# Optimization experiments

Hardware: AMD Instinct MI355X
Metric: run time of the kernel (lower is better)

Reference implementation:

```python
import jax, jax.numpy as jnp
import numpy as np

N, E, D_IN, D, HEADS = 8192, 2048, 256, 256, 4
EPS = 1e-5
NEG = -1e9  # large negative instead of -inf (rows guaranteed non-empty anyway)


def _layernorm(x, g, b):
    mu = jnp.mean(x, axis=-1, keepdims=True)
    var = jnp.mean(jnp.square(x - mu), axis=-1, keepdims=True)
    return (x - mu) * jax.lax.rsqrt(var + EPS) * g + b


def _mha(q_x, kv_x, in_w, in_b, out_w, out_b, mask):
    """torch nn.MultiheadAttention (batch=1, eval) with boolean attn_mask.
    q_x: [Lq, D], kv_x: [Lk, D], mask: [Lq, Lk] True = blocked."""
    hd = D // HEADS
    wq, wk, wv = jnp.split(in_w, 3, axis=0)   # each [D, D]
    bq, bk, bv = jnp.split(in_b, 3, axis=0)
    q = (q_x @ wq.T + bq).reshape(-1, HEADS, hd).transpose(1, 0, 2)  # [h, Lq, hd]
    k = (kv_x @ wk.T + bk).reshape(-1, HEADS, hd).transpose(1, 0, 2)
    v = (kv_x @ wv.T + bv).reshape(-1, HEADS, hd).transpose(1, 0, 2)
    scores = jnp.einsum('hqd,hkd->hqk', q, k) / jnp.sqrt(jnp.asarray(hd, q.dtype))
    scores = jnp.where(mask[None, :, :], NEG, scores)
    attn = jax.nn.softmax(scores, axis=-1)
    out = jnp.einsum('hqk,hkd->hqd', attn, v)           # [h, Lq, hd]
    out = out.transpose(1, 0, 2).reshape(-1, D)          # [Lq, D]
    return out @ out_w.T + out_b


def setup_inputs() -> dict:
    key = jax.random.key(0)
    ks = jax.random.split(key, 12)
    s = 0.02
    x_0 = jax.random.normal(ks[0], (N, D_IN), jnp.float32)
    x_1 = jax.random.normal(ks[1], (E, D_IN), jnp.float32)
    H = (jax.random.uniform(ks[2], (N, E)) < 0.01).astype(jnp.float32)
    H = H.at[jnp.arange(N), jnp.arange(N) % E].set(1.0)
    return {
        'x_0': x_0, 'x_1': x_1, 'incidence_1': H,
        'node_w': jax.random.normal(ks[3], (D, D_IN), jnp.float32) * s,
        'node_b': jnp.zeros((D,), jnp.float32),
        'edge_w': jax.random.normal(ks[4], (D, D_IN), jnp.float32) * s,
        'edge_b': jnp.zeros((D,), jnp.float32),
        'n2e_in_w': jax.random.normal(ks[5], (3 * D, D), jnp.float32) * s,
        'n2e_in_b': jnp.zeros((3 * D,), jnp.float32),
        'n2e_out_w': jax.random.normal(ks[6], (D, D), jnp.float32) * s,
        'n2e_out_b': jnp.zeros((D,), jnp.float32),
        'e2n_in_w': jax.random.normal(ks[7], (3 * D, D), jnp.float32) * s,
        'e2n_in_b': jnp.zeros((3 * D,), jnp.float32),
        'e2n_out_w': jax.random.normal(ks[8], (D, D), jnp.float32) * s,
        'e2n_out_b': jnp.zeros((D,), jnp.float32),
        'norm1_g': jnp.ones((D,), jnp.float32),
        'norm1_b': jnp.zeros((D,), jnp.float32),
        'norm2_g': jnp.ones((D,), jnp.float32),
        'norm2_b': jnp.zeros((D,), jnp.float32),
    }


def reference(x_0, x_1, incidence_1, node_w, node_b, edge_w, edge_b,
              n2e_in_w, n2e_in_b, n2e_out_w, n2e_out_b,
              e2n_in_w, e2n_in_b, e2n_out_w, e2n_out_b,
              norm1_g, norm1_b, norm2_g, norm2_b):
    H = incidence_1                      # [N, E]
    x_0_p = x_0 @ node_w.T + node_b      # [N, D]
    x_1_p = x_1 @ edge_w.T + edge_b      # [E, D]
    # node -> edge: edges query nodes, mask where H.T == 0
    x_1_u = _mha(x_1_p, x_0_p, n2e_in_w, n2e_in_b, n2e_out_w, n2e_out_b,
                 H.T == 0)
    x_1_u = _layernorm(x_1_p + x_1_u, norm1_g, norm1_b)
    # edge -> node: nodes query updated edges, mask where H == 0
    x_0_u = _mha(x_0_p, x_1_u, e2n_in_w, e2n_in_b, e2n_out_w, e2n_out_b,
                 H == 0)
    x_0_u = _layernorm(x_0_p + x_0_u, norm2_g, norm2_b)
    return (x_0_u, x_1_u)
```

## Files before the change

### kernel.cpp

```cpp
#include <hip/hip_runtime.h>
#include <hip/hip_bf16.h>

using bf16 = __hip_bfloat16;
typedef __attribute__((ext_vector_type(4))) float  f32x4;
typedef __attribute__((ext_vector_type(8))) short  s16x8;

#define QSTRIDE 1040
#define ASTRIDE 520
#define BSTRIDE 2064
#define CMAX 256
#define RMAX 128
#define CSTRIDE 16

struct ConvDesc { const float* src[14]; int dstoff[14]; int cnt[14]; };

__global__ __launch_bounds__(256)
void conv_weights(ConvDesc d, bf16* __restrict__ dst, int* __restrict__ cz, int czn)
{
    const int seg = blockIdx.x >> 6;
    const int blk = blockIdx.x & 63;
    if (seg == 14) {
        for (int i = blk * 256 + threadIdx.x; i < czn; i += 64 * 256)
            cz[i] = 0;
        return;
    }
    const float* __restrict__ s = d.src[seg];
    bf16* __restrict__ o = dst + d.dstoff[seg];
    const int n = d.cnt[seg];
    for (int i = blk * 256 + threadIdx.x; i < n; i += 64 * 256)
        o[i] = __float2bfloat16(s[i]);
}

__global__ __launch_bounds__(256)
void build_rows(const float* __restrict__ H, int* __restrict__ row_cnt,
                unsigned short* __restrict__ row_idx)
{
    const int lane = threadIdx.x & 63;
    const int n    = blockIdx.x * 4 + (threadIdx.x >> 6);

    const unsigned long long ltm = (1ull << lane) - 1ull;
    int base = 0;

#pragma unroll
    for (int seg = 0; seg < 8; seg++) {
        f32x4 v = *(const f32x4*)(H + (size_t)n * 2048 + seg * 256 + lane * 4);
        unsigned long long b[4];
#pragma unroll
        for (int j = 0; j < 4; j++) b[j] = __ballot(v[j] != 0.f);

        int pre = 0;
#pragma unroll
        for (int j = 0; j < 4; j++) {
            if (v[j] != 0.f) {
                const int slot = base + pre + (int)__popcll(b[j] & ltm);
                if (slot < RMAX)
                    row_idx[(size_t)n * RMAX + slot] =
                        (unsigned short)(seg * 256 + lane * 4 + j);
            }
            pre += (int)__popcll(b[j]);
        }
        base += pre;
    }
    if (lane == 0) row_cnt[n] = (base < RMAX) ? base : RMAX;
}

__global__ __launch_bounds__(256)
void build_cols(const int* __restrict__ row_cnt,
                const unsigned short* __restrict__ row_idx,
                int* __restrict__ col_cnt, unsigned short* __restrict__ col_idx)
{
    const int g = blockIdx.x * 256 + threadIdx.x;
    const int n = g >> 3;
    const int t = g & 7;
    const int cnt = row_cnt[n];
    for (int i = t; i < cnt; i += 8) {
        const int e = row_idx[(size_t)n * RMAX + i];
        const int s = atomicAdd(&col_cnt[e * CSTRIDE], 1);
        if (s < CMAX) col_idx[(size_t)e * CMAX + s] = (unsigned short)n;
    }
}

__global__ __launch_bounds__(256, 2)
void gemm_proj(const float* __restrict__ X0, const float* __restrict__ X1,
               const bf16* __restrict__ Wc, const bf16* __restrict__ biasc,
               bf16* __restrict__ outB)
{
    __shared__ __align__(16) bf16 As[4 * QSTRIDE];
    __shared__ __align__(16) bf16 Bs[4 * QSTRIDE];

    const int t    = threadIdx.x;
    const int lane = t & 63;
    const int w    = t >> 6;
    const int wm   = (w >> 1) * 64;
    const int wn   = (w & 1) * 64;
    const int bt   = blockIdx.x >> 1;
    const int tn   = (blockIdx.x & 1) * 128;
    if (bt >= 80) return;

    const float* __restrict__ A = (bt < 64) ? X0 : X1;
    const int arow = (bt < 64) ? bt * 128 : (bt - 64) * 128;
    const bf16* __restrict__ W    = Wc    + ((bt < 64) ? 0 : 65536);
    const bf16* __restrict__ bias = biasc + ((bt < 64) ? 0 : 256);
    const int tm = bt * 128;

    f32x4 acc[4][4];
#pragma unroll
    for (int i = 0; i < 4; i++)
#pragma unroll
        for (int j = 0; j < 4; j++)
#pragma unroll
            for (int r = 0; r < 4; r++) acc[i][j][r] = 0.f;

    const int m0 = t >> 2,         q0 = t & 3;
    const int m1 = (t + 256) >> 2, q1 = (t + 256) & 3;
    const int fq = lane >> 4, fr = lane & 15;

    for (int k0 = 0; k0 < 256; k0 += 32) {
        f32x4 a0l = *(const f32x4*)(A + (size_t)(arow + m0) * 256 + k0 + q0 * 8);
        f32x4 a0h = *(const f32x4*)(A + (size_t)(arow + m0) * 256 + k0 + q0 * 8 + 4);
        f32x4 a1l = *(const f32x4*)(A + (size_t)(arow + m1) * 256 + k0 + q1 * 8);
        f32x4 a1h = *(const f32x4*)(A + (size_t)(arow + m1) * 256 + k0 + q1 * 8 + 4);
        union { s16x8 v; bf16 e[8]; } u0, u1;
#pragma unroll
        for (int j = 0; j < 4; j++) {
            u0.e[j] = __float2bfloat16(a0l[j]); u0.e[4 + j] = __float2bfloat16(a0h[j]);
            u1.e[j] = __float2bfloat16(a1l[j]); u1.e[4 + j] = __float2bfloat16(a1h[j]);
        }
        s16x8 sb0 = *(const s16x8*)(W + (size_t)(tn + m0) * 256 + k0 + q0 * 8);
        s16x8 sb1 = *(const s16x8*)(W + (size_t)(tn + m1) * 256 + k0 + q1 * 8);

        __syncthreads();
        *(s16x8*)&As[q0 * QSTRIDE + m0 * 8] = u0.v;
        *(s16x8*)&As[q1 * QSTRIDE + m1 * 8] = u1.v;
        *(s16x8*)&Bs[q0 * QSTRIDE + m0 * 8] = sb0;
        *(s16x8*)&Bs[q1 * QSTRIDE + m1 * 8] = sb1;
        __syncthreads();

        s16x8 af[4], bfv[4];
#pragma unroll
        for (int i = 0; i < 4; i++) {
            af[i]  = *(const s16x8*)&As[fq * QSTRIDE + (wm + i * 16 + fr) * 8];
            bfv[i] = *(const s16x8*)&Bs[fq * QSTRIDE + (wn + i * 16 + fr) * 8];
        }
#pragma unroll
        for (int i = 0; i < 4; i++)
#pragma unroll
            for (int j = 0; j < 4; j++)
                acc[i][j] = __builtin_amdgcn_mfma_f32_16x16x32_bf16(
                    af[i], bfv[j], acc[i][j], 0, 0, 0);
    }

#pragma unroll
    for (int j = 0; j < 4; j++) {
        const int ncol = tn + wn + j * 16 + fr;
        const float bj = __bfloat162float(bias[ncol]);
#pragma unroll
        for (int i = 0; i < 4; i++)
#pragma unroll
            for (int r = 0; r < 4; r++) {
                const int mrow = tm + wm + i * 16 + fq * 4 + r;
                outB[(size_t)mrow * 256 + ncol] = __float2bfloat16(acc[i][j][r] + bj);
            }
    }
}

__global__ __launch_bounds__(256, 2)
void gemm_dual(const bf16* __restrict__ A0, const bf16* __restrict__ W0,
               const bf16* __restrict__ bias0, bf16* __restrict__ out0,
               int N0, int tiles0, int nblk0,
               const bf16* __restrict__ A1, const bf16* __restrict__ W1,
               const bf16* __restrict__ bias1, bf16* __restrict__ out1,
               int N1, int tiles1)
{
    __shared__ __align__(16) bf16 As[4 * QSTRIDE];
    __shared__ __align__(16) bf16 Bs[4 * QSTRIDE];

    const int t    = threadIdx.x;
    const int lane = t & 63;
    const int w    = t >> 6;
    const int wm   = (w >> 1) * 64;
    const int wn   = (w & 1) * 64;

    const bool second = (blockIdx.x >= (unsigned)nblk0);
    const int  bi     = second ? (blockIdx.x - nblk0) : blockIdx.x;
    const bf16* __restrict__ A    = second ? A1 : A0;
    const bf16* __restrict__ W    = second ? W1 : W0;
    const bf16* __restrict__ bias = second ? bias1 : bias0;
    bf16* __restrict__ outB       = second ? out1 : out0;
    const int N      = second ? N1 : N0;
    const int tilesN = second ? tiles1 : tiles0;
    const int tm = (bi / tilesN) * 128;
    const int tn = (bi % tilesN) * 128;

    f32x4 acc[4][4];
#pragma unroll
    for (int i = 0; i < 4; i++)
#pragma unroll
        for (int j = 0; j < 4; j++)
#pragma unroll
            for (int r = 0; r < 4; r++) acc[i][j][r] = 0.f;

    const int m0 = t >> 2,         q0 = t & 3;
    const int m1 = (t + 256) >> 2, q1 = (t + 256) & 3;
    const int fq = lane >> 4, fr = lane & 15;

    for (int k0 = 0; k0 < 256; k0 += 32) {
        s16x8 sa0 = *(const s16x8*)(A + (size_t)(tm + m0) * 256 + k0 + q0 * 8);
        s16x8 sa1 = *(const s16x8*)(A + (size_t)(tm + m1) * 256 + k0 + q1 * 8);
        s16x8 sb0 = *(const s16x8*)(W + (size_t)(tn + m0) * 256 + k0 + q0 * 8);
        s16x8 sb1 = *(const s16x8*)(W + (size_t)(tn + m1) * 256 + k0 + q1 * 8);

        __syncthreads();
        *(s16x8*)&As[q0 * QSTRIDE + m0 * 8] = sa0;
        *(s16x8*)&As[q1 * QSTRIDE + m1 * 8] = sa1;
        *(s16x8*)&Bs[q0 * QSTRIDE + m0 * 8] = sb0;
        *(s16x8*)&Bs[q1 * QSTRIDE + m1 * 8] = sb1;
        __syncthreads();

        s16x8 af[4], bfv[4];
#pragma unroll
        for (int i = 0; i < 4; i++) {
            af[i]  = *(const s16x8*)&As[fq * QSTRIDE + (wm + i * 16 + fr) * 8];
            bfv[i] = *(const s16x8*)&Bs[fq * QSTRIDE + (wn + i * 16 + fr) * 8];
        }
#pragma unroll
        for (int i = 0; i < 4; i++)
#pragma unroll
            for (int j = 0; j < 4; j++)
                acc[i][j] = __builtin_amdgcn_mfma_f32_16x16x32_bf16(
                    af[i], bfv[j], acc[i][j], 0, 0, 0);
    }

#pragma unroll
    for (int j = 0; j < 4; j++) {
        const int ncol = tn + wn + j * 16 + fr;
        const float bj = __bfloat162float(bias[ncol]);
#pragma unroll
        for (int i = 0; i < 4; i++)
#pragma unroll
            for (int r = 0; r < 4; r++) {
                const int mrow = tm + wm + i * 16 + fq * 4 + r;
                outB[(size_t)mrow * N + ncol] = __float2bfloat16(acc[i][j][r] + bj);
            }
    }
}

__global__ __launch_bounds__(256, 2)
void gemm_ln(const bf16* __restrict__ A, const bf16* __restrict__ W,
             const float* __restrict__ biasF, const bf16* __restrict__ xp,
             const float* __restrict__ g, const float* __restrict__ b,
             float* __restrict__ outF, bf16* __restrict__ outB)
{
    __shared__ __align__(16) bf16 As[4 * ASTRIDE];
    __shared__ __align__(16) bf16 Bs[4 * BSTRIDE];
    __shared__ float rs1[64], rs2[64];

    const int t    = threadIdx.x;
    const int lane = t & 63;
    const int w    = t >> 6;
    const int fq   = lane >> 4;
    const int fr   = lane & 15;
    const int tm   = blockIdx.x * 64;

    if (t < 64) { rs1[t] = 0.f; rs2[t] = 0.f; }

    f32x4 acc[4][4];
#pragma unroll
    for (int i = 0; i < 4; i++)
#pragma unroll
        for (int j = 0; j < 4; j++)
#pragma unroll
            for (int r = 0; r < 4; r++) acc[i][j][r] = 0.f;

    const int mA = t >> 2, qA = t & 3;

    for (int k0 = 0; k0 < 256; k0 += 32) {
        s16x8 sa = *(const s16x8*)(A + (size_t)(tm + mA) * 256 + k0 + qA * 8);
        s16x8 sb[4];
#pragma unroll
        for (int s = 0; s < 4; s++)
            sb[s] = *(const s16x8*)(W + (size_t)(mA + 64 * s) * 256 + k0 + qA * 8);

        __syncthreads();
        *(s16x8*)&As[qA * ASTRIDE + mA * 8] = sa;
#pragma unroll
        for (int s = 0; s < 4; s++)
            *(s16x8*)&Bs[qA * BSTRIDE + (mA + 64 * s) * 8] = sb[s];
        __syncthreads();

        s16x8 af[4], bfv[4];
#pragma unroll
        for (int i = 0; i < 4; i++) {
            af[i]  = *(const s16x8*)&As[fq * ASTRIDE + (i * 16 + fr) * 8];
            bfv[i] = *(const s16x8*)&Bs[fq * BSTRIDE + (w * 64 + i * 16 + fr) * 8];
        }
#pragma unroll
        for (int i = 0; i < 4; i++)
#pragma unroll
            for (int j = 0; j < 4; j++)
                acc[i][j] = __builtin_amdgcn_mfma_f32_16x16x32_bf16(
                    af[i], bfv[j], acc[i][j], 0, 0, 0);
    }

    float bj[4], gj[4], bbj[4];
    int colv[4];
#pragma unroll
    for (int j = 0; j < 4; j++) {
        colv[j] = w * 64 + j * 16 + fr;
        bj[j]  = biasF[colv[j]];
        gj[j]  = g[colv[j]];
        bbj[j] = b[colv[j]];
    }

#pragma unroll
    for (int i = 0; i < 4; i++) {
#pragma unroll
        for (int r = 0; r < 4; r++) {
            const int row = i * 16 + fq * 4 + r;
            float t1 = 0.f, t2 = 0.f;
#pragma unroll
            for (int j = 0; j < 4; j++) {
                float v = acc[i][j][r] + bj[j]
                        + __bfloat162float(xp[(size_t)(tm + row) * 256 + colv[j]]);
                acc[i][j][r] = v;
                t1 += v;
                t2 += v * v;
            }
#pragma unroll
            for (int o = 1; o < 16; o <<= 1) {
                t1 += __shfl_xor(t1, o);
                t2 += __shfl_xor(t2, o);
            }
            if (fr == 0) {
                atomicAdd(&rs1[row], t1);
                atomicAdd(&rs2[row], t2);
            }
        }
    }
    __syncthreads();

#pragma unroll
    for (int i = 0; i < 4; i++) {
#pragma unroll
        for (int r = 0; r < 4; r++) {
            const int row = i * 16 + fq * 4 + r;
            const float mu  = rs1[row] * (1.f / 256.f);
            const float var = rs2[row] * (1.f / 256.f) - mu * mu;
            const float rstd = rsqrtf(var + 1e-5f);
#pragma unroll
            for (int j = 0; j < 4; j++) {
                const float y = (acc[i][j][r] - mu) * rstd * gj[j] + bbj[j];
                outF[(size_t)(tm + row) * 256 + colv[j]] = y;
                if (outB) outB[(size_t)(tm + row) * 256 + colv[j]] = __float2bfloat16(y);
            }
        }
    }
}

__global__ __launch_bounds__(256)
void sparse_attn(const bf16* __restrict__ Q, int qs,
                 const bf16* __restrict__ Kb, const bf16* __restrict__ Vb, int kvs,
                 const int* __restrict__ cnts, int cstride,
                 const unsigned short* __restrict__ idx,
                 int lmax, int idxmask, bf16* __restrict__ out)
{
    __shared__ float sc[4][CMAX];
    __shared__ unsigned short nls[CMAX];
    const int qi   = blockIdx.x;
    const int h    = threadIdx.x >> 6;
    const int lane = threadIdx.x & 63;
    const int grp  = lane >> 3;
    const int sub  = lane & 7;

    int n = cnts[(size_t)qi * cstride];
    if (n > lmax) n = lmax;

    if (h == 0)
        for (int i = lane; i < n; i += 64)
            nls[i] = (unsigned short)(((int)idx[(size_t)qi * lmax + i]) & idxmask);
    __syncthreads();

    if (n <= 0) {
        out[(size_t)qi * 256 + h * 64 + lane] = __float2bfloat16(0.f);
        return;
    }

    float qv[8];
    {
        union { f32x4 v; unsigned short u[8]; } qu;
        qu.v = *(const f32x4*)(Q + (size_t)qi * qs + h * 64 + sub * 8);
#pragma unroll
        for (int j = 0; j < 8; j++)
            qv[j] = __uint_as_float(((unsigned)qu.u[j]) << 16) * 0.125f;
    }

    float mx = -1e30f;
#pragma unroll 2
    for (int base = 0; base < n; base += 8) {
        const int i = base + grp;
        float s = -1e30f;
        if (i < n) {
            const int nb = nls[i];
            union { f32x4 v; unsigned short u[8]; } ku;
            ku.v = *(const f32x4*)(Kb + (size_t)nb * kvs + h * 64 + sub * 8);
            float a = 0.f;
#pragma unroll
            for (int j = 0; j < 8; j++)
                a += __uint_as_float(((unsigned)ku.u[j]) << 16) * qv[j];
            a += __shfl_xor(a, 1);
            a += __shfl_xor(a, 2);
            a += __shfl_xor(a, 4);
            if (sub == 0) sc[h][i] = a;
            s = a;
        }
        mx = fmaxf(mx, s);
    }
#pragma unroll
    for (int o = 32; o > 0; o >>= 1) mx = fmaxf(mx, __shfl_xor(mx, o));

    float sum = 0.f;
    for (int base = 0; base < n; base += 64) {
        const int i = base + lane;
        if (i < n) {
            const float p = __expf(sc[h][i] - mx);
            sc[h][i] = p;
            sum += p;
        }
    }
#pragma unroll
    for (int o = 32; o > 0; o >>= 1) sum += __shfl_xor(sum, o);
    const float inv = 1.f / sum;

    float oa[8];
#pragma unroll
    for (int j = 0; j < 8; j++) oa[j] = 0.f;
#pragma unroll 2
    for (int base = 0; base < n; base += 8) {
        const int i = base + grp;
        if (i < n) {
            const float p = sc[h][i];
            const int nb = nls[i];
            union { f32x4 v; unsigned short u[8]; } vu;
            vu.v = *(const f32x4*)(Vb + (size_t)nb * kvs + h * 64 + sub * 8);
#pragma unroll
            for (int j = 0; j < 8; j++)
                oa[j] += p * __uint_as_float(((unsigned)vu.u[j]) << 16);
        }
    }
#pragma unroll
    for (int j = 0; j < 8; j++) {
        oa[j] += __shfl_xor(oa[j], 8);
        oa[j] += __shfl_xor(oa[j], 16);
        oa[j] += __shfl_xor(oa[j], 32);
    }
    if (grp == 0) {
        union { s16x8 v; bf16 e[8]; } ou;
#pragma unroll
        for (int j = 0; j < 8; j++) ou.e[j] = __float2bfloat16(oa[j] * inv);
        *(s16x8*)(out + (size_t)qi * 256 + h * 64 + sub * 8) = ou.v;
    }
}

extern "C" void kernel_launch(void* const* d_in, const int* in_sizes, int n_in,
                              void* d_out, int out_size, void* d_ws, size_t ws_size,
                              hipStream_t stream)
{
    const int N = 8192, E = 2048;

    float* out0 = (float*)d_out;
    float* out1 = (float*)d_out + (size_t)N * 256;

    char* wp = (char*)d_ws;
    auto carve = [&](size_t bytes) { void* p = wp; wp += (bytes + 15) & ~size_t(15); return p; };

    bf16*  wcat    = (bf16*)          carve(657408 * 2);
    int*   col_cnt = (int*)           carve((size_t)E * CSTRIDE * 4);
    int*   row_cnt = (int*)           carve((size_t)N * 4);
    unsigned short* col_idx = (unsigned short*)carve((size_t)E * CMAX * 2);
    unsigned short* row_idx = (unsigned short*)carve((size_t)N * RMAX * 2);
    bf16*  xp01    = (bf16*) carve((size_t)(N + E) * 256 * 2);
    bf16*  kvq     = (bf16*) carve((size_t)N * 768 * 2);
    bf16*  q1      = (bf16*) carve((size_t)E * 256 * 2);
    bf16*  attn1   = (bf16*) carve((size_t)E * 256 * 2);
    bf16*  x1u_b   = (bf16*) carve((size_t)E * 256 * 2);
    bf16*  kv2     = (bf16*) carve((size_t)E * 512 * 2);
    bf16*  attn2   = (bf16*) carve((size_t)N * 256 * 2);

    bf16* x0p = xp01;
    bf16* x1p = xp01 + (size_t)N * 256;

    const int O_PW   = 0;
    const int O_PB   = 131072;
    const int O_KVQ  = 131584;
    const int O_KVQB = 328192;
    const int O_Q1W  = 328960;
    const int O_Q1B  = 394496;
    const int O_KV2W = 394752;
    const int O_KV2B = 525824;
    const int O_O1W  = 526336;
    const int O_O2W  = 591872;

    ConvDesc cd;
    const float* srcs[14] = {
        (const float*)d_in[3], (const float*)d_in[5],
        (const float*)d_in[4], (const float*)d_in[6],
        (const float*)d_in[7] + 65536, (const float*)d_in[11],
        (const float*)d_in[8] + 256,   (const float*)d_in[12],
        (const float*)d_in[7],         (const float*)d_in[8],
        (const float*)d_in[11] + 65536,(const float*)d_in[12] + 256,
        (const float*)d_in[9],         (const float*)d_in[13]
    };
    const int offs[14] = {O_PW, O_PW + 65536, O_PB, O_PB + 256,
                          O_KVQ, O_KVQ + 131072, O_KVQB, O_KVQB + 512,
                          O_Q1W, O_Q1B, O_KV2W, O_KV2B, O_O1W, O_O2W};
    const int cnts[14] = {65536, 65536, 256, 256, 131072, 65536, 512, 256,
                          65536, 256, 131072, 512, 65536, 65536};
    for (int i = 0; i < 14; i++) { cd.src[i] = srcs[i]; cd.dstoff[i] = offs[i]; cd.cnt[i] = cnts[i]; }

    conv_weights<<<15 * 64, 256, 0, stream>>>(cd, wcat, col_cnt, E * CSTRIDE);

    build_rows<<<N / 4, 256, 0, stream>>>((const float*)d_in[2], row_cnt, row_idx);

    build_cols<<<N * 8 / 256, 256, 0, stream>>>(row_cnt, row_idx, col_cnt, col_idx);

    gemm_proj<<<160, 256, 0, stream>>>((const float*)d_in[0], (const float*)d_in[1],
                                       wcat + O_PW, wcat + O_PB, xp01);

    gemm_dual<<<384 + 32, 256, 0, stream>>>(x0p, wcat + O_KVQ, wcat + O_KVQB, kvq,
                                            768, 6, 384,
                                            x1p, wcat + O_Q1W, wcat + O_Q1B, q1,
                                            256, 2);

    sparse_attn<<<E, 256, 0, stream>>>(q1, 256, kvq, kvq + 256, 768,
                                       col_cnt, CSTRIDE, col_idx, CMAX, N - 1, attn1);
    gemm_ln<<<E / 64, 256, 0, stream>>>(attn1, wcat + O_O1W, (const float*)d_in[10],
                                        x1p, (const float*)d_in[15], (const float*)d_in[16],
                                        out1, x1u_b);

    gemm_dual<<<64, 256, 0, stream>>>(x1u_b, wcat + O_KV2W, wcat + O_KV2B, kv2,
                                      512, 4, 64,
                                      nullptr, nullptr, nullptr, nullptr, 256, 2);
    sparse_attn<<<N, 256, 0, stream>>>(kvq + 512, 768, kv2, kv2 + 256, 512,
                                       row_cnt, 1, row_idx, RMAX, E - 1, attn2);
    gemm_ln<<<N / 64, 256, 0, stream>>>(attn2, wcat + O_O2W, (const float*)d_in[14],
                                        x0p, (const float*)d_in[17], (const float*)d_in[18],
                                        out0, nullptr);
}
```

Measured before the change: 256.4 us.

## Fold input projections into attention weights and merge setup kernels

Precomputes composed weights (in_w·node_w etc.) on device so one GEMM directly produces x0_p, K, V, Q from raw fp32 inputs, removing the separate projection GEMM pass and its intermediate round-trip. Merges weight conversion, col_cnt zeroing and row building into one launch, and folds the column build into the big GEMM launch. This cuts the kernel count and one dependent GEMM stage. In exchange it adds a small fp32 weight-composition GEMM per call and rounds the composed weights to bf16, which changes rounding behaviour. The col build runs in the same launch as the GEMM, relying on row data from the previous kernel.

```diff
diff --git a/kernel.cpp b/kernel.cpp
--- a/kernel.cpp
+++ b/kernel.cpp
@@ -12,96 +12,155 @@
 #define RMAX 128
 #define CSTRIDE 16
 
-struct ConvDesc { const float* src[14]; int dstoff[14]; int cnt[14]; };
+#define O_MW0  0
+#define O_MB0  262144
+#define O_MW1  263168
+#define O_MB1  394240
+#define O_KV2W 394752
+#define O_KV2B 525824
+#define O_O1W  526336
+#define O_O2W  591872
+
+struct PrepDesc {
+    const float* aw[4]; const float* pw[4];
+    const float* ab[4]; const float* pb[4];
+    int cdst[4]; int bdst[4];
+    const float* csrc[8]; int coff[8]; int ccnt[8];
+};
 
 __global__ __launch_bounds__(256)
-void conv_weights(ConvDesc d, bf16* __restrict__ dst, int* __restrict__ cz, int czn)
+void prep_front(PrepDesc d, bf16* __restrict__ dst,
+                const float* __restrict__ H, int* __restrict__ col_cnt,
+                int* __restrict__ row_cnt, unsigned short* __restrict__ row_idx)
 {
-    const int seg = blockIdx.x >> 6;
-    const int blk = blockIdx.x & 63;
-    if (seg == 14) {
-        for (int i = blk * 256 + threadIdx.x; i < czn; i += 64 * 256)
-            cz[i] = 0;
+    const int t = threadIdx.x;
+
+    if (blockIdx.x >= 256) {
+        const int b = blockIdx.x - 256;
+        if (t < 16) col_cnt[b * 16 + t] = 0;
+
+        const int lane = t & 63;
+        const int n = b * 4 + (t >> 6);
+        const unsigned long long ltm = (1ull << lane) - 1ull;
+        int base = 0;
+
+#pragma unroll
+        for (int seg = 0; seg < 8; seg++) {
+            f32x4 v = *(const f32x4*)(H + (size_t)n * 2048 + seg * 256 + lane * 4);
+            unsigned long long bm[4];
+#pragma unroll
+            for (int j = 0; j < 4; j++) bm[j] = __ballot(v[j] != 0.f);
+
+            int pre = 0;
+#pragma unroll
+            for (int j = 0; j < 4; j++) {
+                if (v[j] != 0.f) {
+                    const int slot = base + pre + (int)__popcll(bm[j] & ltm);
+                    if (slot < RMAX)
+                        row_idx[(size_t)n * RMAX + slot] =
+                            (unsigned short)(seg * 256 + lane * 4 + j);
+                }
+                pre += (int)__popcll(bm[j]);
+            }
+            base += pre;
+        }
+        if (lane == 0) row_cnt[n] = (base < RMAX) ? base : RMAX;
         return;
     }
-    const float* __restrict__ s = d.src[seg];
-    bf16* __restrict__ o = dst + d.dstoff[seg];
-    const int n = d.cnt[seg];
-    for (int i = blk * 256 + threadIdx.x; i < n; i += 64 * 256)
+
+    if (blockIdx.x < 128) {
+        const int combo = blockIdx.x >> 5;
+        const int i0    = (blockIdx.x & 31) * 8;
+        const float* __restrict__ Aw = d.aw[combo];
+        const float* __restrict__ Bw = d.pw[combo];
+
+        float acc[8];
+#pragma unroll
+        for (int i = 0; i < 8; i++) acc[i] = 0.f;
+
+#pragma unroll 4
+        for (int k = 0; k < 256; k++) {
+            const float bv = Bw[k * 256 + t];
+#pragma unroll
+            for (int i = 0; i < 8; i++)
+                acc[i] += Aw[(i0 + i) * 256 + k] * bv;
+        }
+        bf16* o = dst + d.cdst[combo];
+#pragma unroll
+        for (int i = 0; i < 8; i++)
+            o[(i0 + i) * 256 + t] = __float2bfloat16(acc[i]);
+
+        {
+            const int i  = t >> 5;
+            const int kk = (t & 31) * 8;
+            float s = 0.f;
+#pragma unroll
+            for (int u = 0; u < 8; u++)
+                s += Aw[(i0 + i) * 256 + kk + u] * d.pb[combo][kk + u];
+#pragma unroll
+            for (int o2 = 1; o2 < 32; o2 <<= 1) s += __shfl_xor(s, o2);
+            if ((t & 31) == 0)
+                dst[d.bdst[combo] + i0 + i] =
+                    __float2bfloat16(d.ab[combo][i0 + i] + s);
+        }
+        return;
+    }
+
+    const int seg = (blockIdx.x - 128) >> 4;
+    const int blk = (blockIdx.x - 128) & 15;
+    const float* __restrict__ s = d.csrc[seg];
+    bf16* __restrict__ o = dst + d.coff[seg];
+    const int n = d.ccnt[seg];
+    for (int i = blk * 256 + t; i < n; i += 16 * 256)
         o[i] = __float2bfloat16(s[i]);
 }
 
-__global__ __launch_bounds__(256)
-void build_rows(const float* __restrict__ H, int* __restrict__ row_cnt,
-                unsigned short* __restrict__ row_idx)
-{
-    const int lane = threadIdx.x & 63;
-    const int n    = blockIdx.x * 4 + (threadIdx.x >> 6);
-
-    const unsigned long long ltm = (1ull << lane) - 1ull;
-    int base = 0;
-
-#pragma unroll
-    for (int seg = 0; seg < 8; seg++) {
-        f32x4 v = *(const f32x4*)(H + (size_t)n * 2048 + seg * 256 + lane * 4);
-        unsigned long long b[4];
-#pragma unroll
-        for (int j = 0; j < 4; j++) b[j] = __ballot(v[j] != 0.f);
-
-        int pre = 0;
-#pragma unroll
-        for (int j = 0; j < 4; j++) {
-            if (v[j] != 0.f) {
-                const int slot = base + pre + (int)__popcll(b[j] & ltm);
-                if (slot < RMAX)
-                    row_idx[(size_t)n * RMAX + slot] =
-                        (unsigned short)(seg * 256 + lane * 4 + j);
-            }
-            pre += (int)__popcll(b[j]);
-        }
-        base += pre;
-    }
-    if (lane == 0) row_cnt[n] = (base < RMAX) ? base : RMAX;
-}
-
-__global__ __launch_bounds__(256)
-void build_cols(const int* __restrict__ row_cnt,
-                const unsigned short* __restrict__ row_idx,
-                int* __restrict__ col_cnt, unsigned short* __restrict__ col_idx)
-{
-    const int g = blockIdx.x * 256 + threadIdx.x;
-    const int n = g >> 3;
-    const int t = g & 7;
-    const int cnt = row_cnt[n];
-    for (int i = t; i < cnt; i += 8) {
-        const int e = row_idx[(size_t)n * RMAX + i];
-        const int s = atomicAdd(&col_cnt[e * CSTRIDE], 1);
-        if (s < CMAX) col_idx[(size_t)e * CMAX + s] = (unsigned short)n;
-    }
-}
-
 __global__ __launch_bounds__(256, 2)
-void gemm_proj(const float* __restrict__ X0, const float* __restrict__ X1,
-               const bf16* __restrict__ Wc, const bf16* __restrict__ biasc,
-               bf16* __restrict__ outB)
+void gemm_mega(const float* __restrict__ X0, const float* __restrict__ X1,
+               const bf16* __restrict__ wc,
+               bf16* __restrict__ x0cat, bf16* __restrict__ x1cat,
+               const int* __restrict__ row_cnt,
+               const unsigned short* __restrict__ row_idx,
+               int* __restrict__ col_cnt, unsigned short* __restrict__ col_idx)
 {
     __shared__ __align__(16) bf16 As[4 * QSTRIDE];
     __shared__ __align__(16) bf16 Bs[4 * QSTRIDE];
 
-    const int t    = threadIdx.x;
+    const int t = threadIdx.x;
+
+    if (blockIdx.x >= 576) {
+        const int g = (blockIdx.x - 576) * 256 + t;
+        const int n = g >> 3;
+        const int tt = g & 7;
+        const int cnt = row_cnt[n];
+        for (int i = tt; i < cnt; i += 8) {
+            const int e = row_idx[(size_t)n * RMAX + i];
+            const int s = atomicAdd(&col_cnt[e * CSTRIDE], 1);
+            if (s < CMAX) col_idx[(size_t)e * CMAX + s] = (unsigned short)n;
+        }
+        return;
+    }
+
     const int lane = t & 63;
     const int w    = t >> 6;
     const int wm   = (w >> 1) * 64;
     const int wn   = (w & 1) * 64;
-    const int bt   = blockIdx.x >> 1;
-    const int tn   = (blockIdx.x & 1) * 128;
-    if (bt >= 80) return;
-
-    const float* __restrict__ A = (bt < 64) ? X0 : X1;
-    const int arow = (bt < 64) ? bt * 128 : (bt - 64) * 128;
-    const bf16* __restrict__ W    = Wc    + ((bt < 64) ? 0 : 65536);
-    const bf16* __restrict__ bias = biasc + ((bt < 64) ? 0 : 256);
-    const int tm = bt * 128;
+
+    int rt, ct, ostride;
+    const float* __restrict__ A;
+    const bf16* __restrict__ W;
+    const bf16* __restrict__ bias;
+    bf16* __restrict__ outp;
+    if (blockIdx.x < 512) {
+        rt = blockIdx.x >> 3; ct = blockIdx.x & 7;
+        A = X0; W = wc + O_MW0; bias = wc + O_MB0; outp = x0cat; ostride = 1024;
+    } else {
+        const int b = blockIdx.x - 512;
+        rt = b >> 2; ct = b & 3;
+        A = X1; W = wc + O_MW1; bias = wc + O_MB1; outp = x1cat; ostride = 512;
+    }
+    const int arow = rt * 128;
+    const int tn   = ct * 128;
 
     f32x4 acc[4][4];
 #pragma unroll
@@ -158,8 +217,8 @@
         for (int i = 0; i < 4; i++)
 #pragma unroll
             for (int r = 0; r < 4; r++) {
-                const int mrow = tm + wm + i * 16 + fq * 4 + r;
-                outB[(size_t)mrow * 256 + ncol] = __float2bfloat16(acc[i][j][r] + bj);
+                const int mrow = arow + wm + i * 16 + fq * 4 + r;
+                outp[(size_t)mrow * ostride + ncol] = __float2bfloat16(acc[i][j][r] + bj);
             }
     }
 }
@@ -247,7 +306,7 @@
 
 __global__ __launch_bounds__(256, 2)
 void gemm_ln(const bf16* __restrict__ A, const bf16* __restrict__ W,
-             const float* __restrict__ biasF, const bf16* __restrict__ xp,
+             const float* __restrict__ biasF, const bf16* __restrict__ xp, int xps,
              const float* __restrict__ g, const float* __restrict__ b,
              float* __restrict__ outF, bf16* __restrict__ outB)
 {
@@ -321,7 +380,7 @@
 #pragma unroll
             for (int j = 0; j < 4; j++) {
                 float v = acc[i][j][r] + bj[j]
-                        + __bfloat162float(xp[(size_t)(tm + row) * 256 + colv[j]]);
+                        + __bfloat162float(xp[(size_t)(tm + row) * xps + colv[j]]);
                 acc[i][j][r] = v;
                 t1 += v;
                 t2 += v * v;
@@ -478,71 +537,60 @@
     int*   row_cnt = (int*)           carve((size_t)N * 4);
     unsigned short* col_idx = (unsigned short*)carve((size_t)E * CMAX * 2);
     unsigned short* row_idx = (unsigned short*)carve((size_t)N * RMAX * 2);
-    bf16*  xp01    = (bf16*) carve((size_t)(N + E) * 256 * 2);
-    bf16*  kvq     = (bf16*) carve((size_t)N * 768 * 2);
-    bf16*  q1      = (bf16*) carve((size_t)E * 256 * 2);
+    bf16*  x0cat   = (bf16*) carve((size_t)N * 1024 * 2);
+    bf16*  x1cat   = (bf16*) carve((size_t)E * 512 * 2);
     bf16*  attn1   = (bf16*) carve((size_t)E * 256 * 2);
     bf16*  x1u_b   = (bf16*) carve((size_t)E * 256 * 2);
     bf16*  kv2     = (bf16*) carve((size_t)E * 512 * 2);
     bf16*  attn2   = (bf16*) carve((size_t)N * 256 * 2);
 
-    bf16* x0p = xp01;
-    bf16* x1p = xp01 + (size_t)N * 256;
-
-    const int O_PW   = 0;
-    const int O_PB   = 131072;
-    const int O_KVQ  = 131584;
-    const int O_KVQB = 328192;
-    const int O_Q1W  = 328960;
-    const int O_Q1B  = 394496;
-    const int O_KV2W = 394752;
-    const int O_KV2B = 525824;
-    const int O_O1W  = 526336;
-    const int O_O2W  = 591872;
-
-    ConvDesc cd;
-    const float* srcs[14] = {
-        (const float*)d_in[3], (const float*)d_in[5],
-        (const float*)d_in[4], (const float*)d_in[6],
-        (const float*)d_in[7] + 65536, (const float*)d_in[11],
-        (const float*)d_in[8] + 256,   (const float*)d_in[12],
-        (const float*)d_in[7],         (const float*)d_in[8],
-        (const float*)d_in[11] + 65536,(const float*)d_in[12] + 256,
-        (const float*)d_in[9],         (const float*)d_in[13]
-    };
-    const int offs[14] = {O_PW, O_PW + 65536, O_PB, O_PB + 256,
-                          O_KVQ, O_KVQ + 131072, O_KVQB, O_KVQB + 512,
-                          O_Q1W, O_Q1B, O_KV2W, O_KV2B, O_O1W, O_O2W};
-    const int cnts[14] = {65536, 65536, 256, 256, 131072, 65536, 512, 256,
-                          65536, 256, 131072, 512, 65536, 65536};
-    for (int i = 0; i < 14; i++) { cd.src[i] = srcs[i]; cd.dstoff[i] = offs[i]; cd.cnt[i] = cnts[i]; }
-
-    conv_weights<<<15 * 64, 256, 0, stream>>>(cd, wcat, col_cnt, E * CSTRIDE);
-
-    build_rows<<<N / 4, 256, 0, stream>>>((const float*)d_in[2], row_cnt, row_idx);
-
-    build_cols<<<N * 8 / 256, 256, 0, stream>>>(row_cnt, row_idx, col_cnt, col_idx);
-
-    gemm_proj<<<160, 256, 0, stream>>>((const float*)d_in[0], (const float*)d_in[1],
-                                       wcat + O_PW, wcat + O_PB, xp01);
-
-    gemm_dual<<<384 + 32, 256, 0, stream>>>(x0p, wcat + O_KVQ, wcat + O_KVQB, kvq,
-                                            768, 6, 384,
-                                            x1p, wcat + O_Q1W, wcat + O_Q1B, q1,
-                                            256, 2);
-
-    sparse_attn<<<E, 256, 0, stream>>>(q1, 256, kvq, kvq + 256, 768,
+    const float* nw = (const float*)d_in[3];
+    const float* nb = (const float*)d_in[4];
+    const float* ew = (const float*)d_in[5];
+    const float* eb = (const float*)d_in[6];
+    const float* w1 = (const float*)d_in[7];
+    const float* b1 = (const float*)d_in[8];
+    const float* w2 = (const float*)d_in[11];
+    const float* b2 = (const float*)d_in[12];
+
+    PrepDesc pd;
+    pd.aw[0] = w1 + 65536;  pd.pw[0] = nw; pd.ab[0] = b1 + 256; pd.pb[0] = nb;
+    pd.cdst[0] = O_MW0 + 65536;  pd.bdst[0] = O_MB0 + 256;
+    pd.aw[1] = w1 + 131072; pd.pw[1] = nw; pd.ab[1] = b1 + 512; pd.pb[1] = nb;
+    pd.cdst[1] = O_MW0 + 131072; pd.bdst[1] = O_MB0 + 512;
+    pd.aw[2] = w2;          pd.pw[2] = nw; pd.ab[2] = b2;      pd.pb[2] = nb;
+    pd.cdst[2] = O_MW0 + 196608; pd.bdst[2] = O_MB0 + 768;
+    pd.aw[3] = w1;          pd.pw[3] = ew; pd.ab[3] = b1;      pd.pb[3] = eb;
+    pd.cdst[3] = O_MW1 + 65536;  pd.bdst[3] = O_MB1 + 256;
+    const float* csrc[8] = { nw, ew, w2 + 65536, (const float*)d_in[9],
+                             (const float*)d_in[13], nb, eb, b2 + 256 };
+    const int coff[8] = {O_MW0, O_MW1, O_KV2W, O_O1W, O_O2W, O_MB0, O_MB1, O_KV2B};
+    const int ccnt[8] = {65536, 65536, 131072, 65536, 65536, 256, 256, 512};
+    for (int i = 0; i < 8; i++) { pd.csrc[i] = csrc[i]; pd.coff[i] = coff[i]; pd.ccnt[i] = ccnt[i]; }
+
+    prep_front<<<256 + 2048, 256, 0, stream>>>(pd, wcat, (const float*)d_in[2],
+                                               col_cnt, row_cnt, row_idx);
+
+    gemm_mega<<<576 + 256, 256, 0, stream>>>((const float*)d_in[0],
+                                             (const float*)d_in[1], wcat,
+                                             x0cat, x1cat,
+                                             row_cnt, row_idx, col_cnt, col_idx);
+
+    sparse_attn<<<E, 256, 0, stream>>>(x1cat + 256, 512,
+                                       x0cat + 256, x0cat + 512, 1024,
                                        col_cnt, CSTRIDE, col_idx, CMAX, N - 1, attn1);
     gemm_ln<<<E / 64, 256, 0, stream>>>(attn1, wcat + O_O1W, (const float*)d_in[10],
-                                        x1p, (const float*)d_in[15], (const float*)d_in[16],
+                                        x1cat, 512,
+                                        (const float*)d_in[15], (const float*)d_in[16],
                                         out1, x1u_b);
 
     gemm_dual<<<64, 256, 0, stream>>>(x1u_b, wcat + O_KV2W, wcat + O_KV2B, kv2,
                                       512, 4, 64,
                                       nullptr, nullptr, nullptr, nullptr, 256, 2);
-    sparse_attn<<<N, 256, 0, stream>>>(kvq + 512, 768, kv2, kv2 + 256, 512,
+    sparse_attn<<<N, 256, 0, stream>>>(x0cat + 768, 1024, kv2, kv2 + 256, 512,
                                        row_cnt, 1, row_idx, RMAX, E - 1, attn2);
     gemm_ln<<<N / 64, 256, 0, stream>>>(attn2, wcat + O_O2W, (const float*)d_in[14],
-                                        x0p, (const float*)d_in[17], (const float*)d_in[18],
+                                        x0cat, 1024,
+                                        (const float*)d_in[17], (const float*)d_in[18],
                                         out0, nullptr);
 }
```

Result: slower. 263.4 us (+2.8%).
